# Kernel optimization log

Hardware: AMD Instinct MI355X
Metric: run time of the kernel (lower is better)

## Reference

```python
import jax, jax.numpy as jnp
import numpy as np

EMBED_DIM = 512
NUM_HEADS = 8
HEAD_DIM = EMBED_DIM // NUM_HEADS
BATCH = 2
SEQ = 4096
LN_EPS = 1e-5


def setup_inputs() -> dict:
    key = jax.random.key(0)
    ks = jax.random.split(key, 10)
    s = 1.0 / np.sqrt(EMBED_DIM)
    d = dict(
        x=jax.random.normal(ks[0], (BATCH, SEQ, EMBED_DIM), dtype=jnp.float32),
        wq=jax.random.normal(ks[1], (EMBED_DIM, EMBED_DIM), dtype=jnp.float32) * s,
        bq=jnp.zeros((EMBED_DIM,), jnp.float32),
        wk=jax.random.normal(ks[2], (EMBED_DIM, EMBED_DIM), dtype=jnp.float32) * s,
        bk=jnp.zeros((EMBED_DIM,), jnp.float32),
        wv=jax.random.normal(ks[3], (EMBED_DIM, EMBED_DIM), dtype=jnp.float32) * s,
        bv=jnp.zeros((EMBED_DIM,), jnp.float32),
        wo=jax.random.normal(ks[4], (EMBED_DIM, EMBED_DIM), dtype=jnp.float32) * s,
        bo=jnp.zeros((EMBED_DIM,), jnp.float32),
        ln_g=jnp.ones((EMBED_DIM,), jnp.float32),
        ln_b=jnp.zeros((EMBED_DIM,), jnp.float32),
    )
    return d


def reference(x, wq, bq, wk, bk, wv, bv, wo, bo, ln_g, ln_b):
    B, S, E = x.shape
    H, D = NUM_HEADS, HEAD_DIM
    residual = x
    # QKV projections (weights stored [in, out])
    q = (x @ wq + bq).reshape(B, S, H, D).transpose(0, 2, 1, 3)  # [B,H,S,D]
    k = (x @ wk + bk).reshape(B, S, H, D).transpose(0, 2, 1, 3)
    v = (x @ wv + bv).reshape(B, S, H, D).transpose(0, 2, 1, 3)
    # scaled dot-product attention
    scores = jnp.einsum('bhsd,bhtd->bhst', q, k) / jnp.sqrt(jnp.float32(D))
    attn = jax.nn.softmax(scores, axis=-1)
    ctx = jnp.einsum('bhst,bhtd->bhsd', attn, v)  # [B,H,S,D]
    ctx = ctx.transpose(0, 2, 1, 3).reshape(B, S, E)
    # output projection (dropout=0 in eval) + residual + LayerNorm
    out = ctx @ wo + bo
    y = out + residual
    mu = jnp.mean(y, axis=-1, keepdims=True)
    var = jnp.var(y, axis=-1, keepdims=True)
    y = (y - mu) * jax.lax.rsqrt(var + LN_EPS) * ln_g + ln_b
    return y
```

## Files before the change

kernel.cpp:

```cpp
#include <hip/hip_runtime.h>


typedef unsigned short u16;
typedef unsigned int u32;
typedef short bf16x8 __attribute__((ext_vector_type(8)));
typedef float f32x2 __attribute__((ext_vector_type(2)));
typedef float f32x4 __attribute__((ext_vector_type(4)));
typedef float f32x8 __attribute__((ext_vector_type(8)));
typedef float f32x16 __attribute__((ext_vector_type(16)));
typedef unsigned short u16x4 __attribute__((ext_vector_type(4)));
typedef unsigned int u32x2 __attribute__((ext_vector_type(2)));
typedef unsigned int u32x4 __attribute__((ext_vector_type(4)));

#define S_LEN 4096
#define E_DIM 512
#define H_NUM 8
#define D_DIM 64
#define M_ROWS 8192

#define Q_SCALE 0.18033688011112042f

static __device__ __forceinline__ u16 f2bf(float f) {
    unsigned int u = __float_as_uint(f);
    u += 0x7fffu + ((u >> 16) & 1u);
    return (u16)(u >> 16);
}

static __device__ __forceinline__ u32 cvt_pk_bf16(float a, float b) {
    u32 r;
    asm("v_cvt_pk_bf16_f32 %0, %1, %2" : "=v"(r) : "v"(a), "v"(b));
    return r;
}

#if __has_builtin(__builtin_amdgcn_exp2f)
#define EXP2(x) __builtin_amdgcn_exp2f(x)
#else
static __device__ __forceinline__ float exp2_hw(float x) {
    float r;
    asm volatile("v_exp_f32 %0, %1\n\ts_nop 1" : "=v"(r) : "v"(x));
    return r;
}
#define EXP2(x) exp2_hw(x)
#endif

static __device__ __forceinline__ float vsum16(f32x16 v) {
    f32x8 a = __builtin_shufflevector(v, v, 0, 1, 2, 3, 4, 5, 6, 7) +
              __builtin_shufflevector(v, v, 8, 9, 10, 11, 12, 13, 14, 15);
    f32x4 b = __builtin_shufflevector(a, a, 0, 1, 2, 3) +
              __builtin_shufflevector(a, a, 4, 5, 6, 7);
    f32x2 c = __builtin_shufflevector(b, b, 0, 1) +
              __builtin_shufflevector(b, b, 2, 3);
    return c[0] + c[1];
}

static __device__ __forceinline__ void gload_lds16(const u16* g, u16* l) {
    __builtin_amdgcn_global_load_lds(
        (const __attribute__((address_space(1))) u32*)g,
        (__attribute__((address_space(3))) u32*)l, 16, 0, 0);
}

__global__ __launch_bounds__(256) void cvt_all_k(
    const float* __restrict__ x, u16* __restrict__ xb,
    const float* __restrict__ w0, const float* __restrict__ w1,
    const float* __restrict__ w2, const float* __restrict__ w3,
    u16* __restrict__ o0, u16* __restrict__ o1,
    u16* __restrict__ o2, u16* __restrict__ o3)
{
    __shared__ float fT[64][68];
    if (blockIdx.x < 4096) {
        int i = blockIdx.x * 256 + threadIdx.x;
        float4 v = ((const float4*)x)[i];
        u16x4 o;
        o[0] = f2bf(v.x); o[1] = f2bf(v.y); o[2] = f2bf(v.z); o[3] = f2bf(v.w);
        ((u16x4*)xb)[i] = o;
        return;
    }
    const int g = blockIdx.x - 4096;
    const int which = g >> 6;
    const int tile = g & 63;
    const int k0 = (tile >> 3) * 64, n0 = (tile & 7) * 64;
    const float* w = which == 0 ? w0 : which == 1 ? w1 : which == 2 ? w2 : w3;
    u16* o = which == 0 ? o0 : which == 1 ? o1 : which == 2 ? o2 : o3;
    const int tr = threadIdx.x >> 4, tc = threadIdx.x & 15;
    #pragma unroll
    for (int p = 0; p < 4; p++) {
        const int kr = p * 16 + tr;
        float4 v = *(const float4*)&w[(size_t)(k0 + kr) * 512 + n0 + tc * 4];
        fT[tc * 4 + 0][kr] = v.x;
        fT[tc * 4 + 1][kr] = v.y;
        fT[tc * 4 + 2][kr] = v.z;
        fT[tc * 4 + 3][kr] = v.w;
    }
    __syncthreads();
    #pragma unroll
    for (int p = 0; p < 4; p++) {
        const int nr = p * 16 + tr;
        u16x4 ov;
        ov[0] = f2bf(fT[nr][tc * 4 + 0]);
        ov[1] = f2bf(fT[nr][tc * 4 + 1]);
        ov[2] = f2bf(fT[nr][tc * 4 + 2]);
        ov[3] = f2bf(fT[nr][tc * 4 + 3]);
        *(u16x4*)&o[(size_t)(n0 + nr) * 512 + k0 + tc * 4] = ov;
    }
}

template <int BM, int BN, int MODE>
__global__ __launch_bounds__(256) void gemm_k(
    const u16* __restrict__ A,
    const u16* __restrict__ Wt0, const u16* __restrict__ Wt1,
    const u16* __restrict__ Wt2,
    const float* __restrict__ b0, const float* __restrict__ b1,
    const float* __restrict__ b2,
    u16* __restrict__ q_out, u16* __restrict__ k_out, u16* __restrict__ vt_out,
    const float* __restrict__ resid, float* __restrict__ of32)
{
    constexpr int FM = BM / 32, FN = BN / 32;
    __shared__ __align__(16) u16 Asm[BM * 32];
    __shared__ __align__(16) u16 Bsm[BN * 32];

    const int t = threadIdx.x, wave = t >> 6, lane = t & 63;
    constexpr int nb_per = 512 / BN;
    int sel, bn;
    if (MODE == 0) { sel = blockIdx.x / nb_per; bn = blockIdx.x % nb_per; }
    else           { sel = 0;                   bn = blockIdx.x; }
    const int bm = blockIdx.y;

    const u16* Wt = (MODE == 0) ? (sel == 0 ? Wt0 : (sel == 1 ? Wt1 : Wt2)) : Wt0;
    const float* bias = (MODE == 0) ? (sel == 0 ? b0 : (sel == 1 ? b1 : b2)) : b0;

    const int wm = (wave >> 1) * (BM / 2);
    const int wn = (wave & 1) * (BN / 2);
    const int lrow = lane & 15, kq = (lane >> 4) * 8;

    f32x4 acc[FM][FN];
    #pragma unroll
    for (int i = 0; i < FM; i++)
        #pragma unroll
        for (int j = 0; j < FN; j++)
            acc[i][j] = (f32x4){0.f, 0.f, 0.f, 0.f};

    const u16* Ag = A + (size_t)bm * BM * 512 + (size_t)(t >> 2) * 512 + (t & 3) * 8;
    const u16* Bg = Wt + (size_t)bn * BN * 512 + (size_t)(t >> 2) * 512 + (t & 3) * 8;
    u16* Al = Asm + (size_t)wave * 512;
    u16* Bl = Bsm + (size_t)wave * 512;

    for (int kk = 0; kk < 512; kk += 32) {
        #pragma unroll
        for (int p = 0; p < BM / 32; p++)
            gload_lds16(Ag + (size_t)p * 64 * 512 + kk, Al + p * 2048);
        #pragma unroll
        for (int p = 0; p < BN / 32; p++)
            gload_lds16(Bg + (size_t)p * 64 * 512 + kk, Bl + p * 2048);
        __syncthreads();

        bf16x8 af[FM], bfv[FN];
        #pragma unroll
        for (int i = 0; i < FM; i++)
            af[i] = *(const bf16x8*)&Asm[(wm + i * 16 + lrow) * 32 + kq];
        #pragma unroll
        for (int j = 0; j < FN; j++)
            bfv[j] = *(const bf16x8*)&Bsm[(wn + j * 16 + lrow) * 32 + kq];
        #pragma unroll
        for (int i = 0; i < FM; i++)
            #pragma unroll
            for (int j = 0; j < FN; j++)
                acc[i][j] = __builtin_amdgcn_mfma_f32_16x16x32_bf16(
                    af[i], bfv[j], acc[i][j], 0, 0, 0);
        __syncthreads();
    }

    #pragma unroll
    for (int i = 0; i < FM; i++) {
        #pragma unroll
        for (int j = 0; j < FN; j++) {
            const int col = bn * BN + wn + j * 16 + lrow;
            const float bcol = bias[col];
            const int row0 = bm * BM + wm + i * 16 + (lane >> 4) * 4;
            if (MODE == 0) {
                const int b = row0 >> 12, s0v = row0 & 4095;
                const int h = col >> 6,  d = col & 63;
                if (sel == 2) {
                    u16x4 pk;
                    #pragma unroll
                    for (int q = 0; q < 4; q++)
                        pk[q] = f2bf(acc[i][j][q] + bcol);
                    *(u16x4*)&vt_out[(((size_t)(b * 8 + h)) * 64 + d) * 4096 + s0v] = pk;
                } else {
                    u16* o = (sel == 0) ? q_out : k_out;
                    const float sc = (sel == 0) ? Q_SCALE : 1.0f;
                    #pragma unroll
                    for (int q = 0; q < 4; q++)
                        o[(((size_t)(b * 8 + h)) * 4096 + s0v + q) * 64 + d] =
                            f2bf((acc[i][j][q] + bcol) * sc);
                }
            } else {
                #pragma unroll
                for (int q = 0; q < 4; q++) {
                    const size_t idx = (size_t)(row0 + q) * 512 + col;
                    of32[idx] = acc[i][j][q] + bcol + resid[idx];
                }
            }
        }
    }
}

__global__ __launch_bounds__(512, 2) void attn_k(
    const u16* __restrict__ Q, const u16* __restrict__ K,
    const u16* __restrict__ Vt, u16* __restrict__ ctx)
{
    __shared__ __align__(16) u16 SM[32768];

    const int t = threadIdx.x, w = t >> 6, lane = t & 63;
    const int l31 = lane & 31, hi = lane >> 5;
    const int kh = w >> 2, wl = w & 3;

    const int bid = blockIdx.x;
    const int xcd = bid & 7, j = bid >> 3;
    const int head = xcd * 2 + (j & 1);
    const int qt = j >> 1;

    const u16* Qb = Q + (size_t)head * S_LEN * D_DIM;
    const u16* Kb = K + (size_t)head * S_LEN * D_DIM;
    const u16* Vb = Vt + (size_t)head * D_DIM * S_LEN;
    const int q0w = qt * 256 + wl * 64;

    bf16x8 qfA[4], qfB[4];
    #pragma unroll
    for (int ks = 0; ks < 4; ks++) {
        qfA[ks] = *(const bf16x8*)&Qb[(size_t)(q0w + l31) * 64 + ks * 16 + hi * 8];
        qfB[ks] = *(const bf16x8*)&Qb[(size_t)(q0w + 32 + l31) * 64 + ks * 16 + hi * 8];
    }

    u16* const KH = SM + kh * 16384;
    u16* const VH = KH + 8192;

    const u16* kp[8];
    const u16* vp[8];
    #pragma unroll
    for (int i = 0; i < 8; i++) {
        const int r = (i >> 2) * 32 + l31;
        const int c = (i & 3) * 2 + hi;
        const int phys = r * 8 + (c ^ (r & 7));
        kp[i] = KH + phys * 8;
        vp[i] = VH + phys * 8;
    }

    f32x16 acc0A = {0.f}, acc1A = {0.f}, acc0B = {0.f}, acc1B = {0.f};
    float lA = 0.f, lB = 0.f;
    f32x16 sCA, sCB, sNA, sNB;
    bf16x8 pfA[2], pfB[2];

    const int th = t & 255;
    const int c0 = th, c1 = th + 256;
    const int sr0 = c0 >> 3, sc0 = (c0 & 7) ^ (sr0 & 7);
    const int sr1 = c1 >> 3, sc1 = (c1 & 7) ^ (sr1 & 7);
    const u16* kg0 = Kb + (size_t)(kh * 2048 + sr0) * 64 + sc0 * 8;
    const u16* kg1 = Kb + (size_t)(kh * 2048 + sr1) * 64 + sc1 * 8;
    const u16* vg0 = Vb + (size_t)sr0 * S_LEN + kh * 2048 + sc0 * 8;
    const u16* vg1 = Vb + (size_t)sr1 * S_LEN + kh * 2048 + sc1 * 8;
    u16* const kd0 = KH + wl * 512;
    u16* const kd1 = KH + 2048 + wl * 512;
    u16* const vd0 = VH + wl * 512;
    u16* const vd1 = VH + 2048 + wl * 512;

#define ATTN_STAGE(DST)                                                      \
    {                                                                        \
        gload_lds16(kg0, kd0 + (DST)); gload_lds16(kg1, kd1 + (DST));        \
        gload_lds16(vg0, vd0 + (DST)); gload_lds16(vg1, vd1 + (DST));        \
        kg0 += 4096; kg1 += 4096; vg0 += 64; vg1 += 64;                      \
    }

#define QK_H(BUF, H, SA, SB)                                                 \
    {                                                                        \
        SA = (f32x16){0.f}; SB = (f32x16){0.f};                              \
        __builtin_amdgcn_s_setprio(1);                                       \
        _Pragma("unroll")                                                    \
        for (int ks = 0; ks < 4; ks++) {                                     \
            bf16x8 ka = *(const bf16x8*)(kp[4 * (H) + ks] + (BUF));          \
            SA = __builtin_amdgcn_mfma_f32_32x32x16_bf16(ka, qfA[ks], SA, 0, 0, 0); \
            SB = __builtin_amdgcn_mfma_f32_32x32x16_bf16(ka, qfB[ks], SB, 0, 0, 0); \
        }                                                                    \
        __builtin_amdgcn_s_setprio(0);                                       \
    }

#define EXPPACK_H(SA, SB)                                                    \
    {                                                                        \
        _Pragma("unroll")                                                    \
        for (int e = 0; e < 16; e++) {                                       \
            SA[e] = EXP2(SA[e]); SB[e] = EXP2(SB[e]);                        \
        }                                                                    \
        lA += vsum16(SA);                                                    \
        lB += vsum16(SB);                                                    \
        _Pragma("unroll")                                                    \
        for (int jx = 0; jx < 2; jx++) {                                     \
            const int r0 = jx * 8;                                           \
            u32 ax1 = cvt_pk_bf16(SA[r0 + 0], SA[r0 + 1]);                   \
            u32 ay1 = cvt_pk_bf16(SA[r0 + 4], SA[r0 + 5]);                   \
            asm("v_permlane32_swap_b32 %0, %1" : "+v"(ax1), "+v"(ay1));      \
            u32 ax2 = cvt_pk_bf16(SA[r0 + 2], SA[r0 + 3]);                   \
            u32 ay2 = cvt_pk_bf16(SA[r0 + 6], SA[r0 + 7]);                   \
            asm("v_permlane32_swap_b32 %0, %1" : "+v"(ax2), "+v"(ay2));      \
            u32x4 wva; wva[0] = ax1; wva[1] = ax2; wva[2] = ay1; wva[3] = ay2; \
            pfA[jx] = *(bf16x8*)&wva;                                        \
            u32 bx1 = cvt_pk_bf16(SB[r0 + 0], SB[r0 + 1]);                   \
            u32 by1 = cvt_pk_bf16(SB[r0 + 4], SB[r0 + 5]);                   \
            asm("v_permlane32_swap_b32 %0, %1" : "+v"(bx1), "+v"(by1));      \
            u32 bx2 = cvt_pk_bf16(SB[r0 + 2], SB[r0 + 3]);                   \
            u32 by2 = cvt_pk_bf16(SB[r0 + 6], SB[r0 + 7]);                   \
            asm("v_permlane32_swap_b32 %0, %1" : "+v"(bx2), "+v"(by2));      \
            u32x4 wvb; wvb[0] = bx1; wvb[1] = bx2; wvb[2] = by1; wvb[3] = by2; \
            pfB[jx] = *(bf16x8*)&wvb;                                        \
        }                                                                    \
    }

#define PV_H(BUF, H)                                                         \
    {                                                                        \
        __builtin_amdgcn_s_setprio(1);                                       \
        _Pragma("unroll")                                                    \
        for (int jx = 0; jx < 2; jx++) {                                     \
            bf16x8 va = *(const bf16x8*)(vp[2 * (H) + jx] + (BUF));          \
            bf16x8 vb2 = *(const bf16x8*)(vp[4 + 2 * (H) + jx] + (BUF));     \
            acc0A = __builtin_amdgcn_mfma_f32_32x32x16_bf16(va, pfA[jx], acc0A, 0, 0, 0); \
            acc0B = __builtin_amdgcn_mfma_f32_32x32x16_bf16(va, pfB[jx], acc0B, 0, 0, 0); \
            acc1A = __builtin_amdgcn_mfma_f32_32x32x16_bf16(vb2, pfA[jx], acc1A, 0, 0, 0); \
            acc1B = __builtin_amdgcn_mfma_f32_32x32x16_bf16(vb2, pfB[jx], acc1B, 0, 0, 0); \
        }                                                                    \
        __builtin_amdgcn_s_setprio(0);                                       \
    }

#define BODY(BUF, NBUF, LAST)                                                \
    {                                                                        \
        if (!(LAST)) ATTN_STAGE(NBUF);                                       \
        QK_H(BUF, 1, sNA, sNB);                                              \
        EXPPACK_H(sCA, sCB);                                                 \
        PV_H(BUF, 0);                                                        \
        EXPPACK_H(sNA, sNB);                                                 \
        PV_H(BUF, 1);                                                        \
        __syncthreads();                                                     \
        if (!(LAST)) QK_H(NBUF, 0, sCA, sCB);                                \
    }

    ATTN_STAGE(0);
    __syncthreads();
    QK_H(0, 0, sCA, sCB);

    for (int it = 0; it < 15; ++it) {
        BODY(0, 4096, 0);
        BODY(4096, 0, 0);
    }
    BODY(0, 4096, 0);
    BODY(4096, 0, 1);

    __syncthreads();
    float* const cb = (float*)SM;
    float* const p = cb + (size_t)(wl * 64 + lane) * 34;
    if (kh == 1) {
        #pragma unroll
        for (int e = 0; e < 16; e++) { p[e] = acc0A[e]; p[16 + e] = acc0B[e]; }
        p[32] = lA; p[33] = lB;
    }
    __syncthreads();
    if (kh == 0) {
        #pragma unroll
        for (int e = 0; e < 16; e++) { acc0A[e] += p[e]; acc0B[e] += p[16 + e]; }
        lA += p[32]; lB += p[33];
    }
    __syncthreads();
    if (kh == 1) {
        #pragma unroll
        for (int e = 0; e < 16; e++) { p[e] = acc1A[e]; p[16 + e] = acc1B[e]; }
    }
    __syncthreads();
    if (kh == 0) {
        #pragma unroll
        for (int e = 0; e < 16; e++) { acc1A[e] += p[e]; acc1B[e] += p[16 + e]; }
        lA += __shfl_xor(lA, 32);
        lB += __shfl_xor(lB, 32);

        const int b = head >> 3, h = head & 7;
        const float liA = 1.0f / lA, liB = 1.0f / lB;
        const size_t oA = (size_t)(b * S_LEN + q0w + l31) * 512 + h * 64 + 4 * hi;
        const size_t oB = oA + (size_t)32 * 512;
        #pragma unroll
        for (int rq = 0; rq < 4; rq++) {
            u32x2 wa;
            wa[0] = cvt_pk_bf16(acc0A[4 * rq + 0] * liA, acc0A[4 * rq + 1] * liA);
            wa[1] = cvt_pk_bf16(acc0A[4 * rq + 2] * liA, acc0A[4 * rq + 3] * liA);
            *(u32x2*)&ctx[oA + 8 * rq] = wa;
            wa[0] = cvt_pk_bf16(acc1A[4 * rq + 0] * liA, acc1A[4 * rq + 1] * liA);
            wa[1] = cvt_pk_bf16(acc1A[4 * rq + 2] * liA, acc1A[4 * rq + 3] * liA);
            *(u32x2*)&ctx[oA + 32 + 8 * rq] = wa;
            wa[0] = cvt_pk_bf16(acc0B[4 * rq + 0] * liB, acc0B[4 * rq + 1] * liB);
            wa[1] = cvt_pk_bf16(acc0B[4 * rq + 2] * liB, acc0B[4 * rq + 3] * liB);
            *(u32x2*)&ctx[oB + 8 * rq] = wa;
            wa[0] = cvt_pk_bf16(acc1B[4 * rq + 0] * liB, acc1B[4 * rq + 1] * liB);
            wa[1] = cvt_pk_bf16(acc1B[4 * rq + 2] * liB, acc1B[4 * rq + 3] * liB);
            *(u32x2*)&ctx[oB + 32 + 8 * rq] = wa;
        }
    }
#undef ATTN_STAGE
#undef QK_H
#undef EXPPACK_H
#undef PV_H
#undef BODY
}

__global__ __launch_bounds__(256) void ln_k(const float* __restrict__ y,
                                            const float* __restrict__ g,
                                            const float* __restrict__ beta,
                                            float* __restrict__ out)
{
    const int w = threadIdx.x >> 6, lane = threadIdx.x & 63;
    const size_t row = (size_t)blockIdx.x * 4 + w;
    const float4* yr = (const float4*)(y + row * 512);
    float4 a = yr[lane], b = yr[lane + 64];
    float s  = a.x + a.y + a.z + a.w + b.x + b.y + b.z + b.w;
    float ss = a.x*a.x + a.y*a.y + a.z*a.z + a.w*a.w
             + b.x*b.x + b.y*b.y + b.z*b.z + b.w*b.w;
    #pragma unroll
    for (int o = 1; o < 64; o <<= 1) {
        s  += __shfl_xor(s, o);
        ss += __shfl_xor(ss, o);
    }
    const float mu  = s * (1.0f / 512.0f);
    const float var = ss * (1.0f / 512.0f) - mu * mu;
    const float inv = rsqrtf(var + 1e-5f);
    const float4* g4 = (const float4*)g;
    const float4* b4 = (const float4*)beta;
    float4 ga = g4[lane], gb = g4[lane + 64];
    float4 ba = b4[lane], bb = b4[lane + 64];
    float4 oa, ob;
    oa.x = (a.x - mu) * inv * ga.x + ba.x;
    oa.y = (a.y - mu) * inv * ga.y + ba.y;
    oa.z = (a.z - mu) * inv * ga.z + ba.z;
    oa.w = (a.w - mu) * inv * ga.w + ba.w;
    ob.x = (b.x - mu) * inv * gb.x + bb.x;
    ob.y = (b.y - mu) * inv * gb.y + bb.y;
    ob.z = (b.z - mu) * inv * gb.z + bb.z;
    ob.w = (b.w - mu) * inv * gb.w + bb.w;
    float4* orow = (float4*)(out + row * 512);
    orow[lane] = oa;
    orow[lane + 64] = ob;
}

extern "C" void kernel_launch(void* const* d_in, const int* in_sizes, int n_in,
                              void* d_out, int out_size, void* d_ws, size_t ws_size,
                              hipStream_t stream)
{
    const float* x    = (const float*)d_in[0];
    const float* wq   = (const float*)d_in[1];
    const float* bq   = (const float*)d_in[2];
    const float* wk   = (const float*)d_in[3];
    const float* bk   = (const float*)d_in[4];
    const float* wv   = (const float*)d_in[5];
    const float* bv   = (const float*)d_in[6];
    const float* wo   = (const float*)d_in[7];
    const float* bo   = (const float*)d_in[8];
    const float* ln_g = (const float*)d_in[9];
    const float* ln_b = (const float*)d_in[10];

    char* ws = (char*)d_ws;
    u16* xb   = (u16*)(ws);
    u16* wqt  = (u16*)(ws + 8388608);
    u16* wkt  = (u16*)(ws + 8912896);
    u16* wvt  = (u16*)(ws + 9437184);
    u16* wot  = (u16*)(ws + 9961472);
    u16* Qb   = (u16*)(ws + 10485760);
    u16* Kb   = (u16*)(ws + 18874368);
    u16* Vtb  = (u16*)(ws + 27262976);
    u16* ctxb = (u16*)(ws + 35651584);
    float* yb = (float*)(ws + 10485760);

    cvt_all_k<<<4352, 256, 0, stream>>>(x, xb, wq, wk, wv, wo,
                                        wqt, wkt, wvt, wot);

    gemm_k<128, 128, 0><<<dim3(12, 64), 256, 0, stream>>>(
        xb, wqt, wkt, wvt, bq, bk, bv, Qb, Kb, Vtb, nullptr, nullptr);

    attn_k<<<256, 512, 0, stream>>>(Qb, Kb, Vtb, ctxb);

    gemm_k<128, 64, 2><<<dim3(8, 64), 256, 0, stream>>>(
        ctxb, wot, wot, wot, bo, bo, bo, nullptr, nullptr, nullptr, x, yb);

    ln_k<<<2048, 256, 0, stream>>>(yb, ln_g, ln_b, (float*)d_out);
}
```

Measured before the change: 149.7 us.

## Fuse output projection with residual and LayerNorm; stagger attention wave phases

Replaces the separate output-projection GEMM and LayerNorm kernels with one kernel. Each block computes a full 32x512 row tile, adds bias and residual, and does the row mean and variance reduction through shuffles and shared memory. This removes the fp32 intermediate write and read-back plus one launch, at the cost of fewer, larger blocks that each re-read the whole weight. The QKV GEMM's staging loop now issues BM/64 and BN/64 loads instead of BM/32 and BN/32, which removes redundant and out-of-range LDS copies. In attention, odd waves now run the exp/pack step before the QK step to stagger MFMA and VALU phases across waves.

```diff
diff --git a/kernel.cpp b/kernel.cpp
--- a/kernel.cpp
+++ b/kernel.cpp
@@ -104,15 +104,14 @@
     }
 }
 
-template <int BM, int BN, int MODE>
-__global__ __launch_bounds__(256) void gemm_k(
+template <int BM, int BN>
+__global__ __launch_bounds__(256) void qkv_k(
     const u16* __restrict__ A,
     const u16* __restrict__ Wt0, const u16* __restrict__ Wt1,
     const u16* __restrict__ Wt2,
     const float* __restrict__ b0, const float* __restrict__ b1,
     const float* __restrict__ b2,
-    u16* __restrict__ q_out, u16* __restrict__ k_out, u16* __restrict__ vt_out,
-    const float* __restrict__ resid, float* __restrict__ of32)
+    u16* __restrict__ q_out, u16* __restrict__ k_out, u16* __restrict__ vt_out)
 {
     constexpr int FM = BM / 32, FN = BN / 32;
     __shared__ __align__(16) u16 Asm[BM * 32];
@@ -120,13 +119,11 @@
 
     const int t = threadIdx.x, wave = t >> 6, lane = t & 63;
     constexpr int nb_per = 512 / BN;
-    int sel, bn;
-    if (MODE == 0) { sel = blockIdx.x / nb_per; bn = blockIdx.x % nb_per; }
-    else           { sel = 0;                   bn = blockIdx.x; }
+    const int sel = blockIdx.x / nb_per, bn = blockIdx.x % nb_per;
     const int bm = blockIdx.y;
 
-    const u16* Wt = (MODE == 0) ? (sel == 0 ? Wt0 : (sel == 1 ? Wt1 : Wt2)) : Wt0;
-    const float* bias = (MODE == 0) ? (sel == 0 ? b0 : (sel == 1 ? b1 : b2)) : b0;
+    const u16* Wt = sel == 0 ? Wt0 : (sel == 1 ? Wt1 : Wt2);
+    const float* bias = sel == 0 ? b0 : (sel == 1 ? b1 : b2);
 
     const int wm = (wave >> 1) * (BM / 2);
     const int wn = (wave & 1) * (BN / 2);
@@ -146,10 +143,10 @@
 
     for (int kk = 0; kk < 512; kk += 32) {
         #pragma unroll
-        for (int p = 0; p < BM / 32; p++)
+        for (int p = 0; p < BM / 64; p++)
             gload_lds16(Ag + (size_t)p * 64 * 512 + kk, Al + p * 2048);
         #pragma unroll
-        for (int p = 0; p < BN / 32; p++)
+        for (int p = 0; p < BN / 64; p++)
             gload_lds16(Bg + (size_t)p * 64 * 512 + kk, Bl + p * 2048);
         __syncthreads();
 
@@ -176,29 +173,119 @@
             const int col = bn * BN + wn + j * 16 + lrow;
             const float bcol = bias[col];
             const int row0 = bm * BM + wm + i * 16 + (lane >> 4) * 4;
-            if (MODE == 0) {
-                const int b = row0 >> 12, s0v = row0 & 4095;
-                const int h = col >> 6,  d = col & 63;
-                if (sel == 2) {
-                    u16x4 pk;
-                    #pragma unroll
-                    for (int q = 0; q < 4; q++)
-                        pk[q] = f2bf(acc[i][j][q] + bcol);
-                    *(u16x4*)&vt_out[(((size_t)(b * 8 + h)) * 64 + d) * 4096 + s0v] = pk;
-                } else {
-                    u16* o = (sel == 0) ? q_out : k_out;
-                    const float sc = (sel == 0) ? Q_SCALE : 1.0f;
-                    #pragma unroll
-                    for (int q = 0; q < 4; q++)
-                        o[(((size_t)(b * 8 + h)) * 4096 + s0v + q) * 64 + d] =
-                            f2bf((acc[i][j][q] + bcol) * sc);
-                }
+            const int b = row0 >> 12, s0v = row0 & 4095;
+            const int h = col >> 6,  d = col & 63;
+            if (sel == 2) {
+                u16x4 pk;
+                #pragma unroll
+                for (int q = 0; q < 4; q++)
+                    pk[q] = f2bf(acc[i][j][q] + bcol);
+                *(u16x4*)&vt_out[(((size_t)(b * 8 + h)) * 64 + d) * 4096 + s0v] = pk;
             } else {
+                u16* o = (sel == 0) ? q_out : k_out;
+                const float sc = (sel == 0) ? Q_SCALE : 1.0f;
                 #pragma unroll
-                for (int q = 0; q < 4; q++) {
-                    const size_t idx = (size_t)(row0 + q) * 512 + col;
-                    of32[idx] = acc[i][j][q] + bcol + resid[idx];
-                }
+                for (int q = 0; q < 4; q++)
+                    o[(((size_t)(b * 8 + h)) * 4096 + s0v + q) * 64 + d] =
+                        f2bf((acc[i][j][q] + bcol) * sc);
+            }
+        }
+    }
+}
+
+__global__ __launch_bounds__(256) void oproj_ln_k(
+    const u16* __restrict__ A,
+    const u16* __restrict__ Wt,
+    const float* __restrict__ bo,
+    const float* __restrict__ x,
+    const float* __restrict__ g, const float* __restrict__ beta,
+    float* __restrict__ out)
+{
+    __shared__ __align__(16) u16 Asm[32 * 32];
+    __shared__ __align__(16) u16 Bsm[512 * 32];
+    __shared__ float red[4][32][2];
+
+    const int t = threadIdx.x, wave = t >> 6, lane = t & 63;
+    const int lrow = lane & 15, kq4 = (lane >> 4) * 4, kq = (lane >> 4) * 8;
+    const int wn = wave * 128;
+    const int bm = blockIdx.x;
+
+    f32x4 acc[2][8];
+    #pragma unroll
+    for (int i = 0; i < 2; i++)
+        #pragma unroll
+        for (int j = 0; j < 8; j++)
+            acc[i][j] = (f32x4){0.f, 0.f, 0.f, 0.f};
+
+    const u16* Ag = A + (size_t)bm * 32 * 512 + (size_t)(t >> 2) * 512 + (t & 3) * 8;
+    const u16* Bg = Wt + (size_t)(t >> 2) * 512 + (t & 3) * 8;
+    u16* Al = Asm + (size_t)wave * 512;
+    u16* Bl = Bsm + (size_t)wave * 512;
+
+    for (int kk = 0; kk < 512; kk += 32) {
+        if (t < 128) gload_lds16(Ag + kk, Al);
+        #pragma unroll
+        for (int p = 0; p < 8; p++)
+            gload_lds16(Bg + (size_t)p * 64 * 512 + kk, Bl + p * 2048);
+        __syncthreads();
+
+        bf16x8 af[2], bfv[8];
+        #pragma unroll
+        for (int i = 0; i < 2; i++)
+            af[i] = *(const bf16x8*)&Asm[(i * 16 + lrow) * 32 + kq];
+        #pragma unroll
+        for (int j = 0; j < 8; j++)
+            bfv[j] = *(const bf16x8*)&Bsm[(wn + j * 16 + lrow) * 32 + kq];
+        #pragma unroll
+        for (int i = 0; i < 2; i++)
+            #pragma unroll
+            for (int j = 0; j < 8; j++)
+                acc[i][j] = __builtin_amdgcn_mfma_f32_16x16x32_bf16(
+                    af[i], bfv[j], acc[i][j], 0, 0, 0);
+        __syncthreads();
+    }
+
+    const int grow0 = bm * 32;
+    #pragma unroll
+    for (int i = 0; i < 2; i++) {
+        #pragma unroll
+        for (int q = 0; q < 4; q++) {
+            const int rl = i * 16 + kq4 + q;
+            float s = 0.f, ss = 0.f;
+            #pragma unroll
+            for (int j = 0; j < 8; j++) {
+                const int col = wn + j * 16 + lrow;
+                float v = acc[i][j][q] + bo[col] +
+                          x[(size_t)(grow0 + rl) * 512 + col];
+                acc[i][j][q] = v;
+                s += v; ss += v * v;
+            }
+            s  += __shfl_xor(s, 1);  ss += __shfl_xor(ss, 1);
+            s  += __shfl_xor(s, 2);  ss += __shfl_xor(ss, 2);
+            s  += __shfl_xor(s, 4);  ss += __shfl_xor(ss, 4);
+            s  += __shfl_xor(s, 8);  ss += __shfl_xor(ss, 8);
+            if (lrow == 0) { red[wave][rl][0] = s; red[wave][rl][1] = ss; }
+        }
+    }
+    __syncthreads();
+
+    #pragma unroll
+    for (int i = 0; i < 2; i++) {
+        #pragma unroll
+        for (int q = 0; q < 4; q++) {
+            const int rl = i * 16 + kq4 + q;
+            const float srow = red[0][rl][0] + red[1][rl][0] +
+                               red[2][rl][0] + red[3][rl][0];
+            const float ssrow = red[0][rl][1] + red[1][rl][1] +
+                                red[2][rl][1] + red[3][rl][1];
+            const float mu = srow * (1.0f / 512.0f);
+            const float var = ssrow * (1.0f / 512.0f) - mu * mu;
+            const float inv = rsqrtf(var + 1e-5f);
+            #pragma unroll
+            for (int j = 0; j < 8; j++) {
+                const int col = wn + j * 16 + lrow;
+                out[(size_t)(grow0 + rl) * 512 + col] =
+                    (acc[i][j][q] - mu) * inv * g[col] + beta[col];
             }
         }
     }
@@ -331,8 +418,13 @@
 #define BODY(BUF, NBUF, LAST)                                                \
     {                                                                        \
         if (!(LAST)) ATTN_STAGE(NBUF);                                       \
-        QK_H(BUF, 1, sNA, sNB);                                              \
-        EXPPACK_H(sCA, sCB);                                                 \
+        if (w & 1) {                                                         \
+            EXPPACK_H(sCA, sCB);                                             \
+            QK_H(BUF, 1, sNA, sNB);                                          \
+        } else {                                                             \
+            QK_H(BUF, 1, sNA, sNB);                                          \
+            EXPPACK_H(sCA, sCB);                                             \
+        }                                                                    \
         PV_H(BUF, 0);                                                        \
         EXPPACK_H(sNA, sNB);                                                 \
         PV_H(BUF, 1);                                                        \
@@ -405,44 +497,6 @@
 #undef BODY
 }
 
-__global__ __launch_bounds__(256) void ln_k(const float* __restrict__ y,
-                                            const float* __restrict__ g,
-                                            const float* __restrict__ beta,
-                                            float* __restrict__ out)
-{
-    const int w = threadIdx.x >> 6, lane = threadIdx.x & 63;
-    const size_t row = (size_t)blockIdx.x * 4 + w;
-    const float4* yr = (const float4*)(y + row * 512);
-    float4 a = yr[lane], b = yr[lane + 64];
-    float s  = a.x + a.y + a.z + a.w + b.x + b.y + b.z + b.w;
-    float ss = a.x*a.x + a.y*a.y + a.z*a.z + a.w*a.w
-             + b.x*b.x + b.y*b.y + b.z*b.z + b.w*b.w;
-    #pragma unroll
-    for (int o = 1; o < 64; o <<= 1) {
-        s  += __shfl_xor(s, o);
-        ss += __shfl_xor(ss, o);
-    }
-    const float mu  = s * (1.0f / 512.0f);
-    const float var = ss * (1.0f / 512.0f) - mu * mu;
-    const float inv = rsqrtf(var + 1e-5f);
-    const float4* g4 = (const float4*)g;
-    const float4* b4 = (const float4*)beta;
-    float4 ga = g4[lane], gb = g4[lane + 64];
-    float4 ba = b4[lane], bb = b4[lane + 64];
-    float4 oa, ob;
-    oa.x = (a.x - mu) * inv * ga.x + ba.x;
-    oa.y = (a.y - mu) * inv * ga.y + ba.y;
-    oa.z = (a.z - mu) * inv * ga.z + ba.z;
-    oa.w = (a.w - mu) * inv * ga.w + ba.w;
-    ob.x = (b.x - mu) * inv * gb.x + bb.x;
-    ob.y = (b.y - mu) * inv * gb.y + bb.y;
-    ob.z = (b.z - mu) * inv * gb.z + bb.z;
-    ob.w = (b.w - mu) * inv * gb.w + bb.w;
-    float4* orow = (float4*)(out + row * 512);
-    orow[lane] = oa;
-    orow[lane + 64] = ob;
-}
-
 extern "C" void kernel_launch(void* const* d_in, const int* in_sizes, int n_in,
                               void* d_out, int out_size, void* d_ws, size_t ws_size,
                               hipStream_t stream)
@@ -469,18 +523,15 @@
     u16* Kb   = (u16*)(ws + 18874368);
     u16* Vtb  = (u16*)(ws + 27262976);
     u16* ctxb = (u16*)(ws + 35651584);
-    float* yb = (float*)(ws + 10485760);
 
     cvt_all_k<<<4352, 256, 0, stream>>>(x, xb, wq, wk, wv, wo,
                                         wqt, wkt, wvt, wot);
 
-    gemm_k<128, 128, 0><<<dim3(12, 64), 256, 0, stream>>>(
-        xb, wqt, wkt, wvt, bq, bk, bv, Qb, Kb, Vtb, nullptr, nullptr);
+    qkv_k<128, 128><<<dim3(12, 64), 256, 0, stream>>>(
+        xb, wqt, wkt, wvt, bq, bk, bv, Qb, Kb, Vtb);
 
     attn_k<<<256, 512, 0, stream>>>(Qb, Kb, Vtb, ctxb);
 
-    gemm_k<128, 64, 2><<<dim3(8, 64), 256, 0, stream>>>(
-        ctxb, wot, wot, wot, bo, bo, bo, nullptr, nullptr, nullptr, x, yb);
-
-    ln_k<<<2048, 256, 0, stream>>>(yb, ln_g, ln_b, (float*)d_out);
-}
+    oproj_ln_k<<<256, 256, 0, stream>>>(ctxb, wot, bo, x, ln_g, ln_b,
+                                        (float*)d_out);
+}
```

Measured after the change: 140.2 us. 6.3% less time.
